# Optimization experiments

Measured on AMD Instinct MI355X. Metric: run time of the kernel, lower is better.

Reference implementation:

```python
import jax, jax.numpy as jnp
import numpy as np

NUM_SEGMENTS = 4096
PTS_PER_SEG = 256
N_POINTS = NUM_SEGMENTS * PTS_PER_SEG  # 1,048,576
DESC = 128
N_MID = 4
BN_EPS = 1e-5


def setup_inputs() -> dict:
    key = jax.random.key(0)
    ks = jax.random.split(key, 8)
    points = jax.random.normal(ks[0], (N_POINTS, 2), dtype=jnp.float32)
    # equal-length segments: guarantees every segment non-empty (max is well-defined)
    segment_ids = jnp.repeat(jnp.arange(NUM_SEGMENTS, dtype=jnp.int32), PTS_PER_SEG)
    w_first = jax.random.normal(ks[1], (2, DESC), dtype=jnp.float32) * (1.0 / np.sqrt(2))
    b_first = jax.random.normal(ks[2], (DESC,), dtype=jnp.float32) * 0.01
    mid_gamma = jnp.ones((N_MID, DESC), dtype=jnp.float32)
    mid_beta = jnp.zeros((N_MID, DESC), dtype=jnp.float32)
    mid_w = jax.random.normal(ks[3], (N_MID, DESC, DESC), dtype=jnp.float32) * (1.0 / np.sqrt(DESC))
    mid_b = jax.random.normal(ks[4], (N_MID, DESC), dtype=jnp.float32) * 0.01
    last_gamma = jnp.ones((DESC,), dtype=jnp.float32)
    last_beta = jnp.zeros((DESC,), dtype=jnp.float32)
    return {
        "points": points, "segment_ids": segment_ids,
        "w_first": w_first, "b_first": b_first,
        "mid_gamma": mid_gamma, "mid_beta": mid_beta,
        "mid_w": mid_w, "mid_b": mid_b,
        "last_gamma": last_gamma, "last_beta": last_beta,
    }


def _mish(x):
    return x * jnp.tanh(jax.nn.softplus(x))


def _batchnorm(x, gamma, beta):
    # training-mode BatchNorm1d: batch mean / biased variance over the point dim
    mean = jnp.mean(x, axis=0)
    var = jnp.var(x, axis=0)
    return (x - mean) * jax.lax.rsqrt(var + BN_EPS) * gamma + beta


def reference(points, segment_ids, w_first, b_first, mid_gamma, mid_beta,
              mid_w, mid_b, last_gamma, last_beta):
    x = points @ w_first + b_first                      # [N, desc]
    for i in range(mid_w.shape[0]):                     # [Mish, BN, Linear] * n_mid_mlps
        x = _mish(x)
        x = _batchnorm(x, mid_gamma[i], mid_beta[i])
        x = x @ mid_w[i] + mid_b[i]
    x = _batchnorm(x, last_gamma, last_beta)
    # ragged split-by-length + per-segment max + stack == segment_max
    return jax.ops.segment_max(x, segment_ids, num_segments=NUM_SEGMENTS)
```

## Files before the change

kernel.cpp:

```cpp
#include <hip/hip_runtime.h>
#include <hip/hip_bf16.h>
#include <cstdint>

#define NPTS (1u << 20)
#define CDIM 128
#define NSEG 4096

typedef __attribute__((ext_vector_type(8))) short short8;
typedef __attribute__((ext_vector_type(4))) float f32x4;

#define H_BYTES   268435456ull
#define STATS_OFF H_BYTES
#define STL_OFF   (H_BYTES + 5120)
#define WT_OFF    (H_BYTES + 6144)
#define BP_OFF    (H_BYTES + 6144 + 32768)
#define MAXB_OFF  (H_BYTES + 6144 + 33280)
#define MINB_OFF  (MAXB_OFF + 2097152ull)
#define PART_OFF  (MINB_OFF + 2097152ull)
#define P2_OFF    (PART_OFF + 4194304ull)
#define WS_TOTAL  (P2_OFF + 65536ull)

__device__ __align__(256) unsigned char g_ws[WS_TOTAL];

__device__ __forceinline__ uint32_t bf16rne(float f) {
    uint32_t u = __float_as_uint(f);
    return (u + 0x7fffu + ((u >> 16) & 1u)) >> 16;
}
__device__ __forceinline__ uint32_t pack2(float a, float b) {
    union { __hip_bfloat162 h; uint32_t u; } cv;
    cv.h = __float22bfloat162_rn(make_float2(a, b));
    return cv.u;
}
__device__ __forceinline__ float mish_f(float x) {
    float t = __expf(x);
    float u = t * (t + 2.0f);
    float m = x * u * __builtin_amdgcn_rcpf(u + 2.0f);
    return (x > 15.0f) ? x : m;
}

template <int OP>
__device__ __forceinline__ float block_reduce_128(float (&vals)[8], float* red) {
    int tid = threadIdx.x;
#pragma unroll
    for (int e = 0; e < 8; e++) red[tid * 8 + e] = vals[e];
    __syncthreads();
    float a = (OP == 0) ? 0.f : (OP == 1 ? -3.4e38f : 3.4e38f);
    if (tid < 128) {
        int cg = tid >> 3, e = tid & 7;
#pragma unroll
        for (int r = 0; r < 16; r++) {
            float x = red[(cg + (r << 4)) * 8 + e];
            if (OP == 0) a += x;
            else if (OP == 1) a = fmaxf(a, x);
            else a = fminf(a, x);
        }
    }
    __syncthreads();
    return a;
}

__global__ __launch_bounds__(256) void k_first(const float2* __restrict__ pts,
                                               const float* __restrict__ wf,
                                               const float* __restrict__ bf) {
    uint16_t* hout = (uint16_t*)g_ws;
    float* partials = (float*)(g_ws + PART_OFF);
    int tid = threadIdx.x;
    int colg = tid & 15;
    int rowt = tid >> 4;
    float w0[8], w1[8], bb[8];
#pragma unroll
    for (int e = 0; e < 8; e++) {
        w0[e] = wf[colg * 8 + e];
        w1[e] = wf[128 + colg * 8 + e];
        bb[e] = bf[colg * 8 + e];
    }
    float ssum[8], ssq[8];
#pragma unroll
    for (int e = 0; e < 8; e++) { ssum[e] = 0.f; ssq[e] = 0.f; }

    int base = blockIdx.x * 256;
    for (int p = 0; p < 16; p++) {
        int pi = base + p * 16 + rowt;
        float2 pt = pts[pi];
        float v[8];
#pragma unroll
        for (int e = 0; e < 8; e++) {
            float x = fmaf(pt.x, w0[e], fmaf(pt.y, w1[e], bb[e]));
            v[e] = mish_f(x);
            ssum[e] += v[e];
            ssq[e] += v[e] * v[e];
        }
        uint4 o;
        o.x = pack2(v[0], v[1]); o.y = pack2(v[2], v[3]);
        o.z = pack2(v[4], v[5]); o.w = pack2(v[6], v[7]);
        *(uint4*)(hout + (size_t)pi * CDIM + colg * 8) = o;
    }
    __shared__ float red[2048];
    float s = block_reduce_128<0>(ssum, red);
    float q = block_reduce_128<0>(ssq, red);
    if (tid < 128) {
        partials[(size_t)blockIdx.x * 256 + tid] = s;
        partials[(size_t)blockIdx.x * 256 + 128 + tid] = q;
    }
}

template <int MODE>
__global__ __launch_bounds__(256, 2) void k_gemm() {
    uint16_t* hbuf = (uint16_t*)g_ws;
    const uint16_t* wt = (const uint16_t*)(g_ws + WT_OFF);
    const float* bp = (const float*)(g_ws + BP_OFF);
    float* partials = (float*)(g_ws + PART_OFF);
    float* maxb = (float*)(g_ws + MAXB_OFF);
    float* minb = (float*)(g_ws + MINB_OFF);

    int tid = threadIdx.x;
    int lane = tid & 63;
    int wave = tid >> 6;
    int l15 = lane & 15;
    int l4 = lane >> 4;

    short8 bfrag[8][4];
#pragma unroll
    for (int jb = 0; jb < 8; jb++)
#pragma unroll
        for (int kk = 0; kk < 4; kk++)
            bfrag[jb][kk] = *(const short8*)(wt + (jb * 16 + l15) * CDIM + kk * 32 + l4 * 8);

    float bias_r[8];
#pragma unroll
    for (int e = 0; e < 8; e++) bias_r[e] = bp[(tid & 15) * 8 + e];

    float ssum[8], ssq[8], smax[8], smin[8];
#pragma unroll
    for (int e = 0; e < 8; e++) {
        ssum[e] = 0.f; ssq[e] = 0.f;
        smax[e] = -3.4e38f; smin[e] = 3.4e38f;
    }

    __shared__ float sm[64 * 132];

    size_t rowbase = (size_t)blockIdx.x * 256;

    short8 af[4], afn[4];
    {
        const uint16_t* ap = hbuf + (rowbase + wave * 16 + l15) * CDIM + l4 * 8;
#pragma unroll
        for (int kk = 0; kk < 4; kk++) af[kk] = *(const short8*)(ap + kk * 32);
    }

    for (int g = 0; g < 4; ++g) {
        if (g < 3) {
            const uint16_t* ap = hbuf + (rowbase + (size_t)(g + 1) * 64 + wave * 16 + l15) * CDIM + l4 * 8;
#pragma unroll
            for (int kk = 0; kk < 4; kk++) afn[kk] = *(const short8*)(ap + kk * 32);
        }
        f32x4 acc[8];
#pragma unroll
        for (int jb = 0; jb < 8; jb++) acc[jb] = (f32x4){0.f, 0.f, 0.f, 0.f};
#pragma unroll
        for (int kk = 0; kk < 4; kk++)
#pragma unroll
            for (int jb = 0; jb < 8; jb++)
                acc[jb] = __builtin_amdgcn_mfma_f32_16x16x32_bf16(bfrag[jb][kk], af[kk], acc[jb], 0, 0, 0);

#pragma unroll
        for (int jb = 0; jb < 8; jb++)
            *(f32x4*)&sm[(wave * 16 + l15) * 132 + jb * 16 + l4 * 4] = acc[jb];
        __syncthreads();

        int rt = tid >> 4, cg = tid & 15;
#pragma unroll
        for (int it = 0; it < 4; ++it) {
            int lr = rt + (it << 4);
            const float4* rp = (const float4*)&sm[lr * 132 + cg * 8];
            float4 v0 = rp[0], v1 = rp[1];
            float v[8] = {v0.x, v0.y, v0.z, v0.w, v1.x, v1.y, v1.z, v1.w};
#pragma unroll
            for (int e = 0; e < 8; e++) v[e] += bias_r[e];
            if constexpr (MODE == 0) {
#pragma unroll
                for (int e = 0; e < 8; e++) v[e] = mish_f(v[e]);
                uint4 o;
                o.x = pack2(v[0], v[1]); o.y = pack2(v[2], v[3]);
                o.z = pack2(v[4], v[5]); o.w = pack2(v[6], v[7]);
                *(uint4*)(hbuf + (rowbase + (size_t)g * 64 + lr) * CDIM + cg * 8) = o;
            }
#pragma unroll
            for (int e = 0; e < 8; e++) {
                ssum[e] += v[e];
                ssq[e] += v[e] * v[e];
            }
            if constexpr (MODE == 1) {
#pragma unroll
                for (int e = 0; e < 8; e++) {
                    smax[e] = fmaxf(smax[e], v[e]);
                    smin[e] = fminf(smin[e], v[e]);
                }
            }
        }
        __syncthreads();
        if (g < 3) {
#pragma unroll
            for (int kk = 0; kk < 4; kk++) af[kk] = afn[kk];
        }
    }

    float s = block_reduce_128<0>(ssum, sm);
    float q = block_reduce_128<0>(ssq, sm);
    if (tid < 128) {
        partials[(size_t)blockIdx.x * 256 + tid] = s;
        partials[(size_t)blockIdx.x * 256 + 128 + tid] = q;
    }
    if constexpr (MODE == 1) {
        float mx = block_reduce_128<1>(smax, sm);
        float mn = block_reduce_128<2>(smin, sm);
        if (tid < 128) {
            maxb[(size_t)blockIdx.x * 128 + tid] = mx;
            minb[(size_t)blockIdx.x * 128 + tid] = mn;
        }
    }
}

__global__ __launch_bounds__(256) void k_reduce1() {
    const float* partials = (const float*)(g_ws + PART_OFF);
    float* partial2 = (float*)(g_ws + P2_OFF);
    int c = threadIdx.x;
    int r0 = blockIdx.x * 64;
    float a = 0.f;
    for (int r = 0; r < 64; r++) a += partials[(size_t)(r0 + r) * 256 + c];
    partial2[blockIdx.x * 256 + c] = a;
}
__global__ __launch_bounds__(256) void k_reduce2(int Lout) {
    const float* partial2 = (const float*)(g_ws + P2_OFF);
    float* stats = (float*)(g_ws + STATS_OFF) + Lout * 256;
    int c = threadIdx.x;
    float a = 0.f;
    for (int r = 0; r < 64; r++) a += partial2[r * 256 + c];
    stats[c] = a;
}

__global__ __launch_bounds__(128) void k_fold(int L,
                                              const float* __restrict__ gamma_all, const float* __restrict__ beta_all,
                                              const float* __restrict__ W_all, const float* __restrict__ b_all) {
    const float* gsum = (const float*)(g_ws + STATS_OFF) + L * 256;
    const float* gsq = gsum + 128;
    const float* gamma = gamma_all + L * 128;
    const float* beta = beta_all + L * 128;
    const float* W = W_all + (size_t)L * 16384;
    const float* b = b_all + L * 128;
    uint16_t* wtt = (uint16_t*)(g_ws + WT_OFF);
    float* bpp = (float*)(g_ws + BP_OFF);

    int j = blockIdx.x, k = threadIdx.x;
    float mean = gsum[k] * (1.0f / (float)NPTS);
    float var = gsq[k] * (1.0f / (float)NPTS) - mean * mean;
    float s = gamma[k] * rsqrtf(var + 1e-5f);
    float t = beta[k] - mean * s;
    float w = W[k * 128 + j];
    wtt[j * 128 + k] = (uint16_t)bf16rne(s * w);
    __shared__ float red[128];
    red[k] = t * w;
    __syncthreads();
#pragma unroll
    for (int off = 64; off >= 1; off >>= 1) {
        if (k < off) red[k] += red[k + off];
        __syncthreads();
    }
    if (k == 0) bpp[j] = b[j] + red[0];
}

__global__ void k_lastbn(const float* __restrict__ gamma, const float* __restrict__ beta) {
    const float* gsum = (const float*)(g_ws + STATS_OFF) + 1024;
    const float* gsq = gsum + 128;
    float* st = (float*)(g_ws + STL_OFF);
    int c = threadIdx.x;
    float mean = gsum[c] * (1.0f / (float)NPTS);
    float var = gsq[c] * (1.0f / (float)NPTS) - mean * mean;
    float s = gamma[c] * rsqrtf(var + 1e-5f);
    st[c] = s;
    st[128 + c] = beta[c] - mean * s;
}

__global__ __launch_bounds__(256) void k_final(float* __restrict__ out) {
    const float* maxb = (const float*)(g_ws + MAXB_OFF);
    const float* minb = (const float*)(g_ws + MINB_OFF);
    const float* st = (const float*)(g_ws + STL_OFF);
    int idx = blockIdx.x * 256 + threadIdx.x;
    int c = idx & 127;
    float s = st[c], t = st[128 + c];
    out[idx] = fmaf(s, (s >= 0.f ? maxb[idx] : minb[idx]), t);
}

extern "C" void kernel_launch(void* const* d_in, const int* in_sizes, int n_in,
                              void* d_out, int out_size, void* d_ws, size_t ws_size,
                              hipStream_t stream) {
    const float2* pts = (const float2*)d_in[0];
    const float* wf = (const float*)d_in[2];
    const float* bfirst = (const float*)d_in[3];
    const float* mg = (const float*)d_in[4];
    const float* mb = (const float*)d_in[5];
    const float* mw = (const float*)d_in[6];
    const float* mbi = (const float*)d_in[7];
    const float* lg = (const float*)d_in[8];
    const float* lb = (const float*)d_in[9];
    float* out = (float*)d_out;

    k_first<<<4096, 256, 0, stream>>>(pts, wf, bfirst);
    k_reduce1<<<64, 256, 0, stream>>>();
    k_reduce2<<<1, 256, 0, stream>>>(0);
    for (int L = 0; L < 4; ++L) {
        k_fold<<<128, 128, 0, stream>>>(L, mg, mb, mw, mbi);
        if (L < 3)
            k_gemm<0><<<4096, 256, 0, stream>>>();
        else
            k_gemm<1><<<4096, 256, 0, stream>>>();
        k_reduce1<<<64, 256, 0, stream>>>();
        k_reduce2<<<1, 256, 0, stream>>>(L + 1);
    }
    k_lastbn<<<1, 128, 0, stream>>>(lg, lb);
    k_final<<<2048, 256, 0, stream>>>(out);
}
```

Baseline: 718.8 us.

## Shrink GEMM blocks to 64 rows and fold stats reduction into consumers

```diff
diff --git a/kernel.cpp b/kernel.cpp
--- a/kernel.cpp
+++ b/kernel.cpp
@@ -5,19 +5,19 @@
 #define NPTS (1u << 20)
 #define CDIM 128
 #define NSEG 4096
+#define NBLK 16384
 
 typedef __attribute__((ext_vector_type(8))) short short8;
 typedef __attribute__((ext_vector_type(4))) float f32x4;
 
 #define H_BYTES   268435456ull
-#define STATS_OFF H_BYTES
-#define STL_OFF   (H_BYTES + 5120)
-#define WT_OFF    (H_BYTES + 6144)
-#define BP_OFF    (H_BYTES + 6144 + 32768)
-#define MAXB_OFF  (H_BYTES + 6144 + 33280)
-#define MINB_OFF  (MAXB_OFF + 2097152ull)
-#define PART_OFF  (MINB_OFF + 2097152ull)
-#define P2_OFF    (PART_OFF + 4194304ull)
+#define STL_OFF   H_BYTES
+#define WT_OFF    (STL_OFF + 1024)
+#define BP_OFF    (WT_OFF + 32768)
+#define MAXB_OFF  (BP_OFF + 512)
+#define MINB_OFF  (MAXB_OFF + 8388608ull)
+#define PART_OFF  (MINB_OFF + 8388608ull)
+#define P2_OFF    (PART_OFF + 16777216ull)
 #define WS_TOTAL  (P2_OFF + 65536ull)
 
 __device__ __align__(256) unsigned char g_ws[WS_TOTAL];
@@ -36,27 +36,6 @@
     float u = t * (t + 2.0f);
     float m = x * u * __builtin_amdgcn_rcpf(u + 2.0f);
     return (x > 15.0f) ? x : m;
-}
-
-template <int OP>
-__device__ __forceinline__ float block_reduce_128(float (&vals)[8], float* red) {
-    int tid = threadIdx.x;
-#pragma unroll
-    for (int e = 0; e < 8; e++) red[tid * 8 + e] = vals[e];
-    __syncthreads();
-    float a = (OP == 0) ? 0.f : (OP == 1 ? -3.4e38f : 3.4e38f);
-    if (tid < 128) {
-        int cg = tid >> 3, e = tid & 7;
-#pragma unroll
-        for (int r = 0; r < 16; r++) {
-            float x = red[(cg + (r << 4)) * 8 + e];
-            if (OP == 0) a += x;
-            else if (OP == 1) a = fmaxf(a, x);
-            else a = fminf(a, x);
-        }
-    }
-    __syncthreads();
-    return a;
 }
 
 __global__ __launch_bounds__(256) void k_first(const float2* __restrict__ pts,
@@ -78,8 +57,8 @@
 #pragma unroll
     for (int e = 0; e < 8; e++) { ssum[e] = 0.f; ssq[e] = 0.f; }
 
-    int base = blockIdx.x * 256;
-    for (int p = 0; p < 16; p++) {
+    int base = blockIdx.x * 64;
+    for (int p = 0; p < 4; p++) {
         int pi = base + p * 16 + rowt;
         float2 pt = pts[pi];
         float v[8];
@@ -95,11 +74,23 @@
         o.z = pack2(v[4], v[5]); o.w = pack2(v[6], v[7]);
         *(uint4*)(hout + (size_t)pi * CDIM + colg * 8) = o;
     }
-    __shared__ float red[2048];
-    float s = block_reduce_128<0>(ssum, red);
-    float q = block_reduce_128<0>(ssq, red);
+    __shared__ float red[4096];
+#pragma unroll
+    for (int e = 0; e < 8; e++) {
+        red[tid * 8 + e] = ssum[e];
+        red[2048 + tid * 8 + e] = ssq[e];
+    }
+    __syncthreads();
     if (tid < 128) {
-        partials[(size_t)blockIdx.x * 256 + tid] = s;
+        int cg = tid >> 3, e = tid & 7;
+        float a = 0.f, q = 0.f;
+#pragma unroll
+        for (int r = 0; r < 16; r++) {
+            int i = (cg + (r << 4)) * 8 + e;
+            a += red[i];
+            q += red[2048 + i];
+        }
+        partials[(size_t)blockIdx.x * 256 + tid] = a;
         partials[(size_t)blockIdx.x * 256 + 128 + tid] = q;
     }
 }
@@ -119,6 +110,14 @@
     int l15 = lane & 15;
     int l4 = lane >> 4;
 
+    size_t rowbase = (size_t)blockIdx.x * 64;
+
+    short8 af[4];
+    {
+        const uint16_t* ap = hbuf + (rowbase + wave * 16 + l15) * CDIM + l4 * 8;
+#pragma unroll
+        for (int kk = 0; kk < 4; kk++) af[kk] = *(const short8*)(ap + kk * 32);
+    }
     short8 bfrag[8][4];
 #pragma unroll
     for (int jb = 0; jb < 8; jb++)
@@ -129,6 +128,21 @@
     float bias_r[8];
 #pragma unroll
     for (int e = 0; e < 8; e++) bias_r[e] = bp[(tid & 15) * 8 + e];
+
+    f32x4 acc[8];
+#pragma unroll
+    for (int jb = 0; jb < 8; jb++) acc[jb] = (f32x4){0.f, 0.f, 0.f, 0.f};
+#pragma unroll
+    for (int kk = 0; kk < 4; kk++)
+#pragma unroll
+        for (int jb = 0; jb < 8; jb++)
+            acc[jb] = __builtin_amdgcn_mfma_f32_16x16x32_bf16(bfrag[jb][kk], af[kk], acc[jb], 0, 0, 0);
+
+    __shared__ float sm[64 * 132];
+#pragma unroll
+    for (int jb = 0; jb < 8; jb++)
+        *(f32x4*)&sm[(wave * 16 + l15) * 132 + jb * 16 + l4 * 4] = acc[jb];
+    __syncthreads();
 
     float ssum[8], ssq[8], smax[8], smin[8];
 #pragma unroll
@@ -137,84 +151,67 @@
         smax[e] = -3.4e38f; smin[e] = 3.4e38f;
     }
 
-    __shared__ float sm[64 * 132];
-
-    size_t rowbase = (size_t)blockIdx.x * 256;
-
-    short8 af[4], afn[4];
-    {
-        const uint16_t* ap = hbuf + (rowbase + wave * 16 + l15) * CDIM + l4 * 8;
-#pragma unroll
-        for (int kk = 0; kk < 4; kk++) af[kk] = *(const short8*)(ap + kk * 32);
-    }
-
-    for (int g = 0; g < 4; ++g) {
-        if (g < 3) {
-            const uint16_t* ap = hbuf + (rowbase + (size_t)(g + 1) * 64 + wave * 16 + l15) * CDIM + l4 * 8;
-#pragma unroll
-            for (int kk = 0; kk < 4; kk++) afn[kk] = *(const short8*)(ap + kk * 32);
-        }
-        f32x4 acc[8];
-#pragma unroll
-        for (int jb = 0; jb < 8; jb++) acc[jb] = (f32x4){0.f, 0.f, 0.f, 0.f};
-#pragma unroll
-        for (int kk = 0; kk < 4; kk++)
-#pragma unroll
-            for (int jb = 0; jb < 8; jb++)
-                acc[jb] = __builtin_amdgcn_mfma_f32_16x16x32_bf16(bfrag[jb][kk], af[kk], acc[jb], 0, 0, 0);
-
-#pragma unroll
-        for (int jb = 0; jb < 8; jb++)
-            *(f32x4*)&sm[(wave * 16 + l15) * 132 + jb * 16 + l4 * 4] = acc[jb];
-        __syncthreads();
-
-        int rt = tid >> 4, cg = tid & 15;
-#pragma unroll
-        for (int it = 0; it < 4; ++it) {
-            int lr = rt + (it << 4);
-            const float4* rp = (const float4*)&sm[lr * 132 + cg * 8];
-            float4 v0 = rp[0], v1 = rp[1];
-            float v[8] = {v0.x, v0.y, v0.z, v0.w, v1.x, v1.y, v1.z, v1.w};
-#pragma unroll
-            for (int e = 0; e < 8; e++) v[e] += bias_r[e];
-            if constexpr (MODE == 0) {
-#pragma unroll
-                for (int e = 0; e < 8; e++) v[e] = mish_f(v[e]);
-                uint4 o;
-                o.x = pack2(v[0], v[1]); o.y = pack2(v[2], v[3]);
-                o.z = pack2(v[4], v[5]); o.w = pack2(v[6], v[7]);
-                *(uint4*)(hbuf + (rowbase + (size_t)g * 64 + lr) * CDIM + cg * 8) = o;
+    int rt = tid >> 4, cg = tid & 15;
+#pragma unroll
+    for (int it = 0; it < 4; ++it) {
+        int lr = rt + (it << 4);
+        const float4* rp = (const float4*)&sm[lr * 132 + cg * 8];
+        float4 v0 = rp[0], v1 = rp[1];
+        float v[8] = {v0.x, v0.y, v0.z, v0.w, v1.x, v1.y, v1.z, v1.w};
+#pragma unroll
+        for (int e = 0; e < 8; e++) v[e] += bias_r[e];
+        if constexpr (MODE == 0) {
+#pragma unroll
+            for (int e = 0; e < 8; e++) v[e] = mish_f(v[e]);
+            uint4 o;
+            o.x = pack2(v[0], v[1]); o.y = pack2(v[2], v[3]);
+            o.z = pack2(v[4], v[5]); o.w = pack2(v[6], v[7]);
+            *(uint4*)(hbuf + (rowbase + lr) * CDIM + cg * 8) = o;
+        }
+#pragma unroll
+        for (int e = 0; e < 8; e++) {
+            ssum[e] += v[e];
+            ssq[e] += v[e] * v[e];
+        }
+        if constexpr (MODE == 1) {
+#pragma unroll
+            for (int e = 0; e < 8; e++) {
+                smax[e] = fmaxf(smax[e], v[e]);
+                smin[e] = fminf(smin[e], v[e]);
             }
-#pragma unroll
-            for (int e = 0; e < 8; e++) {
-                ssum[e] += v[e];
-                ssq[e] += v[e] * v[e];
+        }
+    }
+    __syncthreads();
+
+#pragma unroll
+    for (int e = 0; e < 8; e++) {
+        sm[tid * 8 + e] = ssum[e];
+        sm[2048 + tid * 8 + e] = ssq[e];
+    }
+    if constexpr (MODE == 1) {
+#pragma unroll
+        for (int e = 0; e < 8; e++) {
+            sm[4096 + tid * 8 + e] = smax[e];
+            sm[6144 + tid * 8 + e] = smin[e];
+        }
+    }
+    __syncthreads();
+    if (tid < 128) {
+        int cg2 = tid >> 3, e = tid & 7;
+        float a = 0.f, q = 0.f, mx = -3.4e38f, mn = 3.4e38f;
+#pragma unroll
+        for (int r = 0; r < 16; r++) {
+            int i = (cg2 + (r << 4)) * 8 + e;
+            a += sm[i];
+            q += sm[2048 + i];
+            if (MODE == 1) {
+                mx = fmaxf(mx, sm[4096 + i]);
+                mn = fminf(mn, sm[6144 + i]);
             }
-            if constexpr (MODE == 1) {
-#pragma unroll
-                for (int e = 0; e < 8; e++) {
-                    smax[e] = fmaxf(smax[e], v[e]);
-                    smin[e] = fminf(smin[e], v[e]);
-                }
-            }
-        }
-        __syncthreads();
-        if (g < 3) {
-#pragma unroll
-            for (int kk = 0; kk < 4; kk++) af[kk] = afn[kk];
-        }
-    }
-
-    float s = block_reduce_128<0>(ssum, sm);
-    float q = block_reduce_128<0>(ssq, sm);
-    if (tid < 128) {
-        partials[(size_t)blockIdx.x * 256 + tid] = s;
+        }
+        partials[(size_t)blockIdx.x * 256 + tid] = a;
         partials[(size_t)blockIdx.x * 256 + 128 + tid] = q;
-    }
-    if constexpr (MODE == 1) {
-        float mx = block_reduce_128<1>(smax, sm);
-        float mn = block_reduce_128<2>(smin, sm);
-        if (tid < 128) {
+        if (MODE == 1) {
             maxb[(size_t)blockIdx.x * 128 + tid] = mx;
             minb[(size_t)blockIdx.x * 128 + tid] = mn;
         }
@@ -225,60 +222,70 @@
     const float* partials = (const float*)(g_ws + PART_OFF);
     float* partial2 = (float*)(g_ws + P2_OFF);
     int c = threadIdx.x;
-    int r0 = blockIdx.x * 64;
+    int r0 = blockIdx.x * 256;
     float a = 0.f;
-    for (int r = 0; r < 64; r++) a += partials[(size_t)(r0 + r) * 256 + c];
+    for (int r = 0; r < 256; r++) a += partials[(size_t)(r0 + r) * 256 + c];
     partial2[blockIdx.x * 256 + c] = a;
 }
-__global__ __launch_bounds__(256) void k_reduce2(int Lout) {
-    const float* partial2 = (const float*)(g_ws + P2_OFF);
-    float* stats = (float*)(g_ws + STATS_OFF) + Lout * 256;
-    int c = threadIdx.x;
-    float a = 0.f;
-    for (int r = 0; r < 64; r++) a += partial2[r * 256 + c];
-    stats[c] = a;
-}
-
-__global__ __launch_bounds__(128) void k_fold(int L,
+
+__global__ __launch_bounds__(256) void k_fold(int L,
                                               const float* __restrict__ gamma_all, const float* __restrict__ beta_all,
                                               const float* __restrict__ W_all, const float* __restrict__ b_all) {
-    const float* gsum = (const float*)(g_ws + STATS_OFF) + L * 256;
-    const float* gsq = gsum + 128;
+    const float* partial2 = (const float*)(g_ws + P2_OFF);
+    uint16_t* wtt = (uint16_t*)(g_ws + WT_OFF);
+    float* bpp = (float*)(g_ws + BP_OFF);
     const float* gamma = gamma_all + L * 128;
     const float* beta = beta_all + L * 128;
     const float* W = W_all + (size_t)L * 16384;
     const float* b = b_all + L * 128;
-    uint16_t* wtt = (uint16_t*)(g_ws + WT_OFF);
-    float* bpp = (float*)(g_ws + BP_OFF);
-
-    int j = blockIdx.x, k = threadIdx.x;
-    float mean = gsum[k] * (1.0f / (float)NPTS);
-    float var = gsq[k] * (1.0f / (float)NPTS) - mean * mean;
-    float s = gamma[k] * rsqrtf(var + 1e-5f);
-    float t = beta[k] - mean * s;
-    float w = W[k * 128 + j];
-    wtt[j * 128 + k] = (uint16_t)bf16rne(s * w);
-    __shared__ float red[128];
-    red[k] = t * w;
+
+    __shared__ float sstats[256];
+    __shared__ float sv[128], tv[128], red[128];
+    int t = threadIdx.x;
+    float a = 0.f;
+    for (int r = 0; r < 64; r++) a += partial2[r * 256 + t];
+    sstats[t] = a;
+    __syncthreads();
+    if (t < 128) {
+        float mean = sstats[t] * (1.0f / (float)NPTS);
+        float var = sstats[128 + t] * (1.0f / (float)NPTS) - mean * mean;
+        float s = gamma[t] * rsqrtf(var + 1e-5f);
+        sv[t] = s;
+        tv[t] = beta[t] - mean * s;
+    }
+    __syncthreads();
+    int j = blockIdx.x;
+    if (t < 128) {
+        float w = W[t * 128 + j];
+        wtt[j * 128 + t] = (uint16_t)bf16rne(sv[t] * w);
+        red[t] = tv[t] * w;
+    }
     __syncthreads();
 #pragma unroll
     for (int off = 64; off >= 1; off >>= 1) {
-        if (k < off) red[k] += red[k + off];
+        if (t < off) red[t] += red[t + off];
         __syncthreads();
     }
-    if (k == 0) bpp[j] = b[j] + red[0];
-}
-
-__global__ void k_lastbn(const float* __restrict__ gamma, const float* __restrict__ beta) {
-    const float* gsum = (const float*)(g_ws + STATS_OFF) + 1024;
-    const float* gsq = gsum + 128;
+    if (t == 0) bpp[j] = b[j] + red[0];
+}
+
+__global__ __launch_bounds__(256) void k_lastbn(const float* __restrict__ gamma,
+                                                const float* __restrict__ beta) {
+    const float* partial2 = (const float*)(g_ws + P2_OFF);
     float* st = (float*)(g_ws + STL_OFF);
-    int c = threadIdx.x;
-    float mean = gsum[c] * (1.0f / (float)NPTS);
-    float var = gsq[c] * (1.0f / (float)NPTS) - mean * mean;
-    float s = gamma[c] * rsqrtf(var + 1e-5f);
-    st[c] = s;
-    st[128 + c] = beta[c] - mean * s;
+    __shared__ float sstats[256];
+    int t = threadIdx.x;
+    float a = 0.f;
+    for (int r = 0; r < 64; r++) a += partial2[r * 256 + t];
+    sstats[t] = a;
+    __syncthreads();
+    if (t < 128) {
+        float mean = sstats[t] * (1.0f / (float)NPTS);
+        float var = sstats[128 + t] * (1.0f / (float)NPTS) - mean * mean;
+        float s = gamma[t] * rsqrtf(var + 1e-5f);
+        st[t] = s;
+        st[128 + t] = beta[t] - mean * s;
+    }
 }
 
 __global__ __launch_bounds__(256) void k_final(float* __restrict__ out) {
@@ -287,8 +294,19 @@
     const float* st = (const float*)(g_ws + STL_OFF);
     int idx = blockIdx.x * 256 + threadIdx.x;
     int c = idx & 127;
+    int seg = idx >> 7;
     float s = st[c], t = st[128 + c];
-    out[idx] = fmaf(s, (s >= 0.f ? maxb[idx] : minb[idx]), t);
+    float r;
+    if (s >= 0.f) {
+        r = maxb[(size_t)(seg * 4) * 128 + c];
+#pragma unroll
+        for (int i = 1; i < 4; i++) r = fmaxf(r, maxb[(size_t)(seg * 4 + i) * 128 + c]);
+    } else {
+        r = minb[(size_t)(seg * 4) * 128 + c];
+#pragma unroll
+        for (int i = 1; i < 4; i++) r = fminf(r, minb[(size_t)(seg * 4 + i) * 128 + c]);
+    }
+    out[idx] = fmaf(s, r, t);
 }
 
 extern "C" void kernel_launch(void* const* d_in, const int* in_sizes, int n_in,
@@ -305,18 +323,16 @@
     const float* lb = (const float*)d_in[9];
     float* out = (float*)d_out;
 
-    k_first<<<4096, 256, 0, stream>>>(pts, wf, bfirst);
+    k_first<<<NBLK, 256, 0, stream>>>(pts, wf, bfirst);
     k_reduce1<<<64, 256, 0, stream>>>();
-    k_reduce2<<<1, 256, 0, stream>>>(0);
     for (int L = 0; L < 4; ++L) {
-        k_fold<<<128, 128, 0, stream>>>(L, mg, mb, mw, mbi);
+        k_fold<<<128, 256, 0, stream>>>(L, mg, mb, mw, mbi);
         if (L < 3)
-            k_gemm<0><<<4096, 256, 0, stream>>>();
+            k_gemm<0><<<NBLK, 256, 0, stream>>>();
         else
-            k_gemm<1><<<4096, 256, 0, stream>>>();
+            k_gemm<1><<<NBLK, 256, 0, stream>>>();
         k_reduce1<<<64, 256, 0, stream>>>();
-        k_reduce2<<<1, 256, 0, stream>>>(L + 1);
-    }
-    k_lastbn<<<1, 128, 0, stream>>>(lg, lb);
+    }
+    k_lastbn<<<256, 256, 0, stream>>>(lg, lb);
     k_final<<<2048, 256, 0, stream>>>(out);
 }
```

Result: slower. 1.390 ms (+93.4%).
